# Kernel tuning notes

Hardware: AMD Instinct MI355X
Metric: run time of the kernel (lower is better)

## Reference

```python
import jax, jax.numpy as jnp
import numpy as np

N_NODES = 100000
N_EDGES = 3200000
SIGMA_REF = 0.07
T_REF = 293.15
DSIGMA_DT = -0.0001
PHI_THRESH = 0.3
EPS = 1e-8


def compute_gradient(T, pos, edge_index):
    """Edge-based finite-difference gradient, scatter-reduced to nodes.

    grad_T[i] = mean over incoming edges (src->i) of
                (T[src]-T[i]) * (pos[src]-pos[i]) / |pos[src]-pos[i]|^2
    """
    src, dst = edge_index[0], edge_index[1]
    dT = T[src] - T[dst]                         # [E]
    dpos = pos[src] - pos[dst]                   # [E,3]
    dist2 = jnp.sum(dpos * dpos, axis=-1) + EPS  # [E]
    contrib = (dT / dist2)[:, None] * dpos       # [E,3]
    num = jax.ops.segment_sum(contrib, dst, num_segments=N_NODES)            # [N,3]
    cnt = jax.ops.segment_sum(jnp.ones_like(dT), dst, num_segments=N_NODES)  # [N]
    return num / jnp.maximum(cnt, 1.0)[:, None]


def setup_inputs() -> dict:
    key = jax.random.key(0)
    k1, k2, k3 = jax.random.split(key, 3)
    x = jax.random.normal(k1, (N_NODES, 9), dtype=jnp.float32)
    pos = jax.random.normal(k2, (N_NODES, 3), dtype=jnp.float32)
    edge_index = jax.random.randint(k3, (2, N_EDGES), 0, N_NODES, dtype=jnp.int64)
    return {"x": x, "pos": pos, "edge_index": edge_index}


def reference(x, pos, edge_index):
    T = x[:, 3]
    phi = x[:, 8]
    grad_T = compute_gradient(T, pos, edge_index)          # [N,3]
    force = DSIGMA_DT * grad_T                             # [N,3]
    interface_mask = (jnp.abs(phi) < PHI_THRESH).astype(force.dtype)
    return force * interface_mask[:, None]
```

## Files before the change

### kernel.cpp

```cpp
#include <hip/hip_runtime.h>

#define N_NODES 100000
#define N_EDGES 3200000
#define NVEC    (N_EDGES / 4)

#define S_LOG2  7
#define S       (1 << S_LOG2)
#define NPART   ((N_NODES + S - 1) / S)
#define NPB     832
#define GSTRIDE 16

#define EPB     6144
#define NB      ((N_EDGES + EPB - 1) / EPB)
#define CAP     4992
#define KPT     10

constexpr float DSIGMA_DT  = -0.0001f;
constexpr float PHI_THRESH = 0.3f;
constexpr float EPS        = 1e-8f;

__global__ __launch_bounds__(512, 4) void bin_kernel(
        const int4* __restrict__ ei4,
        const float* __restrict__ x,
        const float* __restrict__ pos,
        float4* __restrict__ posT,
        int* __restrict__ gcur,
        int* __restrict__ buckets) {
    __shared__ unsigned long long l64[EPB];
    __shared__ int hist[NPB], lofs[NPB];
    __shared__ int baseg[NPART];
    const int tid = threadIdx.x;

    {
        const int per = (N_NODES + NB - 1) / NB;
        const int lo = blockIdx.x * per;
        const int hi = min(lo + per, N_NODES);
        for (int i = lo + tid; i < hi; i += 512)
            posT[i] = make_float4(pos[3 * i], pos[3 * i + 1], pos[3 * i + 2],
                                  x[9 * i + 3]);
    }

    const int ebase = blockIdx.x * EPB;
    const int n  = min(EPB, N_EDGES - ebase);
    const int nv = n >> 2;
    const int4* __restrict__ src4 = ei4 + (ebase >> 2);
    const int4* __restrict__ dst4 = ei4 + NVEC + (ebase >> 2);

    for (int i = tid; i < NPB; i += 512) hist[i] = 0;
    __syncthreads();

    int4 rs[3], rd[3];
    unsigned short rk[12];
#pragma unroll
    for (int k = 0; k < 3; ++k) {
        int v = tid + k * 512;
        if (v < nv) {
            rs[k] = src4[v];
            rd[k] = dst4[v];
            rk[4 * k + 0] = (unsigned short)atomicAdd(&hist[rd[k].x >> S_LOG2], 1);
            rk[4 * k + 1] = (unsigned short)atomicAdd(&hist[rd[k].y >> S_LOG2], 1);
            rk[4 * k + 2] = (unsigned short)atomicAdd(&hist[rd[k].z >> S_LOG2], 1);
            rk[4 * k + 3] = (unsigned short)atomicAdd(&hist[rd[k].w >> S_LOG2], 1);
        }
    }
    __syncthreads();

    if (tid < 64) {
        int carry = 0;
        for (int b = 0; b < NPB; b += 64) {
            int v = hist[b + tid];
            int orig = v;
#pragma unroll
            for (int d = 1; d < 64; d <<= 1) {
                int t = __shfl_up(v, d, 64);
                if (tid >= d) v += t;
            }
            lofs[b + tid] = carry + v - orig;
            carry += __shfl(v, 63, 64);
        }
    }
    __syncthreads();
    for (int i = tid; i < NPART; i += 512)
        baseg[i] = atomicAdd(&gcur[i * GSTRIDE], hist[i]);
    __syncthreads();

#pragma unroll
    for (int k = 0; k < 3; ++k) {
        int v = tid + k * 512;
        if (v < nv) {
#pragma unroll
            for (int j = 0; j < 4; ++j) {
                int dk = j == 0 ? rd[k].x : j == 1 ? rd[k].y : j == 2 ? rd[k].z : rd[k].w;
                int sk = j == 0 ? rs[k].x : j == 1 ? rs[k].y : j == 2 ? rs[k].z : rs[k].w;
                int bin = dk >> S_LOG2;
                int pos = lofs[bin] + (int)rk[4 * k + j];
                l64[pos] = ((unsigned long long)(unsigned)bin << 32)
                         | (unsigned)((sk << S_LOG2) | (dk & (S - 1)));
            }
        }
    }
    __syncthreads();

    for (int i = tid; i < n; i += 512) {
        unsigned long long t = l64[i];
        int b = (int)(t >> 32);
        int e = (int)(unsigned)t;
        int pos = baseg[b] + (i - lofs[b]);
        if (pos < CAP) buckets[(size_t)b * CAP + pos] = e;
    }
}

__global__ __launch_bounds__(512, 8) void part_kernel(
        const int* __restrict__ gcur,
        const int* __restrict__ buckets,
        const float4* __restrict__ posT,
        const float* __restrict__ x,
        float* __restrict__ out) {
    __shared__ int S2[CAP];
    __shared__ int hist[S], base[S];
    __shared__ float4 ploc[S];
    const int p = blockIdx.x, tid = threadIdx.x;
    const int lo = p << S_LOG2;

    if (tid < S) {
        hist[tid] = 0;
        int node = lo + tid;
        ploc[tid] = (node < N_NODES) ? posT[node] : make_float4(0.f, 0.f, 0.f, 0.f);
    }
    const int len = min(gcur[p * GSTRIDE], CAP);
    const int* __restrict__ bp = buckets + (size_t)p * CAP;
    __syncthreads();

    int ent[KPT];
    unsigned short prk[KPT];
#pragma unroll
    for (int k = 0; k < KPT; ++k) {
        int i = tid + k * 512;
        ent[k] = 0;
        if (i < len) {
            ent[k] = bp[i];
            prk[k] = (unsigned short)atomicAdd(&hist[ent[k] & (S - 1)], 1);
        }
    }
    __syncthreads();

    if (tid < 64) {
        int carry = 0;
        for (int b = 0; b < S; b += 64) {
            int v = hist[b + tid];
            int orig = v;
#pragma unroll
            for (int d = 1; d < 64; d <<= 1) {
                int t = __shfl_up(v, d, 64);
                if (tid >= d) v += t;
            }
            base[b + tid] = carry + v - orig;
            carry += __shfl(v, 63, 64);
        }
    }
    __syncthreads();

#pragma unroll
    for (int k = 0; k < KPT; ++k) {
        int i = tid + k * 512;
        if (i < len)
            S2[base[ent[k] & (S - 1)] + (int)prk[k]] = ent[k] >> S_LOG2;
    }
    __syncthreads();

    const int r = tid >> 2, q = tid & 3;
    const int node = lo + r;
    const int nseg = hist[r];
    const int b0 = base[r];
    float4 b = ploc[r];
    float ax = 0.f, ay = 0.f, az = 0.f;
    for (int j = b0 + q; j < b0 + nseg; j += 4) {
        float4 a = posT[S2[j]];
        float px = a.x - b.x, py = a.y - b.y, pz = a.z - b.z;
        float dT = a.w - b.w;
        float w  = dT / (px * px + py * py + pz * pz + EPS);
        ax += w * px; ay += w * py; az += w * pz;
    }
    ax += __shfl_down(ax, 2, 64); ax += __shfl_down(ax, 1, 64);
    ay += __shfl_down(ay, 2, 64); ay += __shfl_down(ay, 1, 64);
    az += __shfl_down(az, 2, 64); az += __shfl_down(az, 1, 64);
    if (q == 0 && node < N_NODES) {
        float phi = x[node * 9 + 8];
        float cn = nseg > 1 ? (float)nseg : 1.0f;
        float m = (fabsf(phi) < PHI_THRESH) ? (DSIGMA_DT / cn) : 0.0f;
        out[3 * node]     = m * ax;
        out[3 * node + 1] = m * ay;
        out[3 * node + 2] = m * az;
    }
}

__global__ void prep_kernel(const float* __restrict__ x,
                            const float* __restrict__ pos,
                            float4* __restrict__ posT) {
    int i = blockIdx.x * blockDim.x + threadIdx.x;
    if (i < N_NODES)
        posT[i] = make_float4(pos[3 * i], pos[3 * i + 1], pos[3 * i + 2],
                              x[9 * i + 3]);
}

__global__ void edge_scatter_atomic_kernel(const int* __restrict__ ei,
                                           const float4* __restrict__ posT,
                                           float4* __restrict__ accum) {
    int e = blockIdx.x * blockDim.x + threadIdx.x;
    if (e >= N_EDGES) return;
    int s = ei[e];
    int d = ei[N_EDGES + e];
    float4 a = posT[s];
    float4 b = posT[d];
    float px = a.x - b.x, py = a.y - b.y, pz = a.z - b.z;
    float dT = a.w - b.w;
    float w  = dT / (px * px + py * py + pz * pz + EPS);
    float* ac = (float*)&accum[d];
    atomicAdd(ac,     w * px);
    atomicAdd(ac + 1, w * py);
    atomicAdd(ac + 2, w * pz);
    atomicAdd(ac + 3, 1.0f);
}

__global__ void finalize_accum_kernel(const float* __restrict__ x,
                                      const float4* __restrict__ accum,
                                      float* __restrict__ out) {
    int i = blockIdx.x * blockDim.x + threadIdx.x;
    if (i >= N_NODES) return;
    float4 a = accum[i];
    float phi = x[i * 9 + 8];
    float cn = a.w > 1.0f ? a.w : 1.0f;
    float m = (fabsf(phi) < PHI_THRESH) ? (DSIGMA_DT / cn) : 0.0f;
    out[3 * i]     = m * a.x;
    out[3 * i + 1] = m * a.y;
    out[3 * i + 2] = m * a.z;
}

extern "C" void kernel_launch(void* const* d_in, const int* in_sizes, int n_in,
                              void* d_out, int out_size, void* d_ws, size_t ws_size,
                              hipStream_t stream) {
    const float* x   = (const float*)d_in[0];
    const float* pos = (const float*)d_in[1];
    const int*   ei  = (const int*)d_in[2];
    float* out = (float*)d_out;

    const size_t posT_b = (size_t)N_NODES * sizeof(float4);
    const size_t gcur_b = 65536;
    const size_t buck_b = (size_t)NPART * CAP * sizeof(int);

    char* w = (char*)d_ws;
    float4* posT    = (float4*)w;
    int*    gcur    = (int*)(w + posT_b);
    int*    buckets = (int*)(w + posT_b + gcur_b);

    const size_t need_full = posT_b + gcur_b + buck_b;

    const int B = 256;

    if (ws_size >= need_full) {
        hipMemsetAsync(gcur, 0, gcur_b, stream);
        bin_kernel<<<NB, 512, 0, stream>>>((const int4*)ei, x, pos, posT, gcur, buckets);
        part_kernel<<<NPART, 512, 0, stream>>>(gcur, buckets, posT, x, out);
    } else {
        float4* accum = (float4*)(w + posT_b);
        prep_kernel<<<(N_NODES + B - 1) / B, B, 0, stream>>>(x, pos, posT);
        hipMemsetAsync(accum, 0, (size_t)N_NODES * sizeof(float4), stream);
        edge_scatter_atomic_kernel<<<(N_EDGES + B - 1) / B, B, 0, stream>>>(ei, posT, accum);
        finalize_accum_kernel<<<(N_NODES + B - 1) / B, B, 0, stream>>>(x, accum, out);
    }
}
```

Before: 131.1 us.

## Replace per-partition counting sort with LDS float atomic accumulation

In part_kernel, the per-block counting sort (histogram, scan, scatter to shared memory, then a segmented reduction over 4 lanes per node) is replaced by direct accumulation. Each thread processes edges in bucket order and does shared-memory float atomicAdds into per-node x/y/z/count accumulators. This removes several barriers, the scan, the KPT register arrays and the 20KB of shared sorted storage, which should help occupancy. In exchange it pays four LDS atomics per edge with possible contention on hot nodes, and the float summation order is no longer deterministic.

```diff
diff --git a/kernel.cpp b/kernel.cpp
--- a/kernel.cpp
+++ b/kernel.cpp
@@ -13,7 +13,6 @@
 #define EPB     6144
 #define NB      ((N_EDGES + EPB - 1) / EPB)
 #define CAP     4992
-#define KPT     10
 
 constexpr float DSIGMA_DT  = -0.0001f;
 constexpr float PHI_THRESH = 0.3f;
@@ -116,81 +115,50 @@
         const float4* __restrict__ posT,
         const float* __restrict__ x,
         float* __restrict__ out) {
-    __shared__ int S2[CAP];
-    __shared__ int hist[S], base[S];
+    __shared__ float acc[4 * (S + 1)];
     __shared__ float4 ploc[S];
     const int p = blockIdx.x, tid = threadIdx.x;
     const int lo = p << S_LOG2;
 
     if (tid < S) {
-        hist[tid] = 0;
         int node = lo + tid;
         ploc[tid] = (node < N_NODES) ? posT[node] : make_float4(0.f, 0.f, 0.f, 0.f);
     }
+    if (tid < 4 * (S + 1)) acc[tid] = 0.f;
     const int len = min(gcur[p * GSTRIDE], CAP);
     const int* __restrict__ bp = buckets + (size_t)p * CAP;
     __syncthreads();
 
-    int ent[KPT];
-    unsigned short prk[KPT];
-#pragma unroll
-    for (int k = 0; k < KPT; ++k) {
-        int i = tid + k * 512;
-        ent[k] = 0;
-        if (i < len) {
-            ent[k] = bp[i];
-            prk[k] = (unsigned short)atomicAdd(&hist[ent[k] & (S - 1)], 1);
-        }
-    }
-    __syncthreads();
-
-    if (tid < 64) {
-        int carry = 0;
-        for (int b = 0; b < S; b += 64) {
-            int v = hist[b + tid];
-            int orig = v;
-#pragma unroll
-            for (int d = 1; d < 64; d <<= 1) {
-                int t = __shfl_up(v, d, 64);
-                if (tid >= d) v += t;
-            }
-            base[b + tid] = carry + v - orig;
-            carry += __shfl(v, 63, 64);
-        }
-    }
-    __syncthreads();
-
-#pragma unroll
-    for (int k = 0; k < KPT; ++k) {
-        int i = tid + k * 512;
-        if (i < len)
-            S2[base[ent[k] & (S - 1)] + (int)prk[k]] = ent[k] >> S_LOG2;
-    }
-    __syncthreads();
-
-    const int r = tid >> 2, q = tid & 3;
-    const int node = lo + r;
-    const int nseg = hist[r];
-    const int b0 = base[r];
-    float4 b = ploc[r];
-    float ax = 0.f, ay = 0.f, az = 0.f;
-    for (int j = b0 + q; j < b0 + nseg; j += 4) {
-        float4 a = posT[S2[j]];
+    for (int i = tid; i < len; i += 512) {
+        int v = bp[i];
+        int d = v & (S - 1);
+        int s = v >> S_LOG2;
+        float4 a = posT[s];
+        float4 b = ploc[d];
         float px = a.x - b.x, py = a.y - b.y, pz = a.z - b.z;
         float dT = a.w - b.w;
         float w  = dT / (px * px + py * py + pz * pz + EPS);
-        ax += w * px; ay += w * py; az += w * pz;
-    }
-    ax += __shfl_down(ax, 2, 64); ax += __shfl_down(ax, 1, 64);
-    ay += __shfl_down(ay, 2, 64); ay += __shfl_down(ay, 1, 64);
-    az += __shfl_down(az, 2, 64); az += __shfl_down(az, 1, 64);
-    if (q == 0 && node < N_NODES) {
-        float phi = x[node * 9 + 8];
-        float cn = nseg > 1 ? (float)nseg : 1.0f;
-        float m = (fabsf(phi) < PHI_THRESH) ? (DSIGMA_DT / cn) : 0.0f;
-        out[3 * node]     = m * ax;
-        out[3 * node + 1] = m * ay;
-        out[3 * node + 2] = m * az;
+        atomicAdd(&acc[d],               w * px);
+        atomicAdd(&acc[(S + 1) + d],     w * py);
+        atomicAdd(&acc[2 * (S + 1) + d], w * pz);
+        atomicAdd(&acc[3 * (S + 1) + d], 1.0f);
+    }
+    __syncthreads();
+
+    if (tid < S) {
+        int node = lo + tid;
+        if (node < N_NODES) {
+            float ax = acc[tid];
+            float ay = acc[(S + 1) + tid];
+            float az = acc[2 * (S + 1) + tid];
+            float aw = acc[3 * (S + 1) + tid];
+            float phi = x[node * 9 + 8];
+            float cn = aw > 1.0f ? aw : 1.0f;
+            float m = (fabsf(phi) < PHI_THRESH) ? (DSIGMA_DT / cn) : 0.0f;
+            out[3 * node]     = m * ax;
+            out[3 * node + 1] = m * ay;
+            out[3 * node + 2] = m * az;
+        }
     }
 }
 
```

New measurement: 195.2 us. +48.9%, slower.

## Replace global atomic bucketing with per-chunk sorted runs and offset table

Applied to the files above, without the earlier changes.

The binning kernel no longer reserves space in global per-partition buckets with atomics. Each edge chunk instead writes its locally bin-sorted entries contiguously, plus a table of per-partition offsets. The partition kernel, now 256 nodes per block with 1024 threads, gathers its segment from every chunk through that table. This removes the memset and the global atomic contention, and the second kernel's scattered writes become coalesced. In exchange there are many small scattered segment reads per partition, heavy register arrays that may spill, and a fixed cap of 64 edges per chunk segment.

```diff
diff --git a/kernel.cpp b/kernel.cpp
--- a/kernel.cpp
+++ b/kernel.cpp
@@ -4,43 +4,43 @@
 #define N_EDGES 3200000
 #define NVEC    (N_EDGES / 4)
 
-#define S_LOG2  7
+#define S_LOG2  8
 #define S       (1 << S_LOG2)
 #define NPART   ((N_NODES + S - 1) / S)
-#define NPB     832
-#define GSTRIDE 16
+#define NPB     448
+#define TROW    (NPART + 1)
 
 #define EPB     6144
-#define NB      ((N_EDGES + EPB - 1) / EPB)
-#define CAP     4992
-#define KPT     10
+#define NCH     ((N_EDGES + EPB - 1) / EPB)
+#define CAP     9216
+#define PIT     9
 
 constexpr float DSIGMA_DT  = -0.0001f;
 constexpr float PHI_THRESH = 0.3f;
 constexpr float EPS        = 1e-8f;
 
-__global__ __launch_bounds__(512, 4) void bin_kernel(
+__global__ __launch_bounds__(512, 8) void bin_kernel(
         const int4* __restrict__ ei4,
         const float* __restrict__ x,
         const float* __restrict__ pos,
         float4* __restrict__ posT,
-        int* __restrict__ gcur,
-        int* __restrict__ buckets) {
-    __shared__ unsigned long long l64[EPB];
+        int* __restrict__ tab,
+        int* __restrict__ buckets2) {
+    __shared__ int lbuf[EPB];
     __shared__ int hist[NPB], lofs[NPB];
-    __shared__ int baseg[NPART];
     const int tid = threadIdx.x;
+    const int c   = blockIdx.x;
 
     {
-        const int per = (N_NODES + NB - 1) / NB;
-        const int lo = blockIdx.x * per;
+        const int per = (N_NODES + NCH - 1) / NCH;
+        const int lo = c * per;
         const int hi = min(lo + per, N_NODES);
         for (int i = lo + tid; i < hi; i += 512)
             posT[i] = make_float4(pos[3 * i], pos[3 * i + 1], pos[3 * i + 2],
                                   x[9 * i + 3]);
     }
 
-    const int ebase = blockIdx.x * EPB;
+    const int ebase = c * EPB;
     const int n  = min(EPB, N_EDGES - ebase);
     const int nv = n >> 2;
     const int4* __restrict__ src4 = ei4 + (ebase >> 2);
@@ -80,9 +80,6 @@
         }
     }
     __syncthreads();
-    for (int i = tid; i < NPART; i += 512)
-        baseg[i] = atomicAdd(&gcur[i * GSTRIDE], hist[i]);
-    __syncthreads();
 
 #pragma unroll
     for (int k = 0; k < 3; ++k) {
@@ -93,26 +90,22 @@
                 int dk = j == 0 ? rd[k].x : j == 1 ? rd[k].y : j == 2 ? rd[k].z : rd[k].w;
                 int sk = j == 0 ? rs[k].x : j == 1 ? rs[k].y : j == 2 ? rs[k].z : rs[k].w;
                 int bin = dk >> S_LOG2;
-                int pos = lofs[bin] + (int)rk[4 * k + j];
-                l64[pos] = ((unsigned long long)(unsigned)bin << 32)
-                         | (unsigned)((sk << S_LOG2) | (dk & (S - 1)));
-            }
-        }
-    }
-    __syncthreads();
-
-    for (int i = tid; i < n; i += 512) {
-        unsigned long long t = l64[i];
-        int b = (int)(t >> 32);
-        int e = (int)(unsigned)t;
-        int pos = baseg[b] + (i - lofs[b]);
-        if (pos < CAP) buckets[(size_t)b * CAP + pos] = e;
-    }
-}
-
-__global__ __launch_bounds__(512, 8) void part_kernel(
-        const int* __restrict__ gcur,
-        const int* __restrict__ buckets,
+                lbuf[lofs[bin] + (int)rk[4 * k + j]] =
+                    (sk << S_LOG2) | (dk & (S - 1));
+            }
+        }
+    }
+    __syncthreads();
+
+    for (int p = tid; p < NPART; p += 512) tab[c * TROW + p] = lofs[p];
+    if (tid == 0) tab[c * TROW + NPART] = n;
+    for (int i = tid; i < n; i += 512)
+        buckets2[ebase + i] = lbuf[i];
+}
+
+__global__ __launch_bounds__(1024, 4) void part_kernel(
+        const int* __restrict__ tab,
+        const int* __restrict__ buckets2,
         const float4* __restrict__ posT,
         const float* __restrict__ x,
         float* __restrict__ out) {
@@ -127,19 +120,30 @@
         int node = lo + tid;
         ploc[tid] = (node < N_NODES) ? posT[node] : make_float4(0.f, 0.f, 0.f, 0.f);
     }
-    const int len = min(gcur[p * GSTRIDE], CAP);
-    const int* __restrict__ bp = buckets + (size_t)p * CAP;
-    __syncthreads();
-
-    int ent[KPT];
-    unsigned short prk[KPT];
-#pragma unroll
-    for (int k = 0; k < KPT; ++k) {
-        int i = tid + k * 512;
-        ent[k] = 0;
-        if (i < len) {
-            ent[k] = bp[i];
-            prk[k] = (unsigned short)atomicAdd(&hist[ent[k] & (S - 1)], 1);
+    __syncthreads();
+
+    const int g = tid >> 4, j = tid & 15;
+    int ent[PIT][4];
+    unsigned short prk[PIT][4];
+    int cnt[PIT];
+#pragma unroll
+    for (int it = 0; it < PIT; ++it) {
+        const int c = it * 64 + g;
+        cnt[it] = 0;
+        if (c < NCH) {
+            int o0 = tab[c * TROW + p];
+            int o1 = tab[c * TROW + p + 1];
+            cnt[it] = o1 - o0;
+            const int* seg = buckets2 + c * EPB + o0;
+#pragma unroll
+            for (int r = 0; r < 4; ++r) {
+                int idx = j + 16 * r;
+                if (idx < cnt[it]) {
+                    int e = seg[idx];
+                    ent[it][r] = e;
+                    prk[it][r] = (unsigned short)atomicAdd(&hist[e & (S - 1)], 1);
+                }
+            }
         }
     }
     __syncthreads();
@@ -161,21 +165,28 @@
     __syncthreads();
 
 #pragma unroll
-    for (int k = 0; k < KPT; ++k) {
-        int i = tid + k * 512;
-        if (i < len)
-            S2[base[ent[k] & (S - 1)] + (int)prk[k]] = ent[k] >> S_LOG2;
-    }
-    __syncthreads();
-
-    const int r = tid >> 2, q = tid & 3;
-    const int node = lo + r;
-    const int nseg = hist[r];
-    const int b0 = base[r];
-    float4 b = ploc[r];
+    for (int it = 0; it < PIT; ++it) {
+#pragma unroll
+        for (int r = 0; r < 4; ++r) {
+            int idx = j + 16 * r;
+            if (idx < cnt[it]) {
+                int e = ent[it][r];
+                int pos = base[e & (S - 1)] + (int)prk[it][r];
+                if (pos < CAP) S2[pos] = e >> S_LOG2;
+            }
+        }
+    }
+    __syncthreads();
+
+    const int rr = tid >> 2, q = tid & 3;
+    const int node = lo + rr;
+    const int nseg = hist[rr];
+    const int b0 = base[rr];
+    const int jend = min(b0 + nseg, CAP);
+    float4 b = ploc[rr];
     float ax = 0.f, ay = 0.f, az = 0.f;
-    for (int j = b0 + q; j < b0 + nseg; j += 4) {
-        float4 a = posT[S2[j]];
+    for (int jj = b0 + q; jj < jend; jj += 4) {
+        float4 a = posT[S2[jj]];
         float px = a.x - b.x, py = a.y - b.y, pz = a.z - b.z;
         float dT = a.w - b.w;
         float w  = dT / (px * px + py * py + pz * pz + EPS);
@@ -245,22 +256,21 @@
     float* out = (float*)d_out;
 
     const size_t posT_b = (size_t)N_NODES * sizeof(float4);
-    const size_t gcur_b = 65536;
-    const size_t buck_b = (size_t)NPART * CAP * sizeof(int);
+    const size_t tab_b  = ((size_t)NCH * TROW * sizeof(int) + 255) & ~255ull;
+    const size_t buck_b = (size_t)NCH * EPB * sizeof(int);
 
     char* w = (char*)d_ws;
-    float4* posT    = (float4*)w;
-    int*    gcur    = (int*)(w + posT_b);
-    int*    buckets = (int*)(w + posT_b + gcur_b);
-
-    const size_t need_full = posT_b + gcur_b + buck_b;
+    float4* posT     = (float4*)w;
+    int*    tab      = (int*)(w + posT_b);
+    int*    buckets2 = (int*)(w + posT_b + tab_b);
+
+    const size_t need_full = posT_b + tab_b + buck_b;
 
     const int B = 256;
 
     if (ws_size >= need_full) {
-        hipMemsetAsync(gcur, 0, gcur_b, stream);
-        bin_kernel<<<NB, 512, 0, stream>>>((const int4*)ei, x, pos, posT, gcur, buckets);
-        part_kernel<<<NPART, 512, 0, stream>>>(gcur, buckets, posT, x, out);
+        bin_kernel<<<NCH, 512, 0, stream>>>((const int4*)ei, x, pos, posT, tab, buckets2);
+        part_kernel<<<NPART, 1024, 0, stream>>>(tab, buckets2, posT, x, out);
     } else {
         float4* accum = (float4*)(w + posT_b);
         prep_kernel<<<(N_NODES + B - 1) / B, B, 0, stream>>>(x, pos, posT);
```

New measurement: 121.2 us. 7.5% less time.
